# Optimization experiments

Measured on AMD Instinct MI355X. Metric: run time of the kernel, lower is better.

## Reference

```python
import jax, jax.numpy as jnp
import numpy as np

N = 50000      # nodes
E = 800000     # edges
F_NODE = 64
PE = 16
F_EDGE = 16
H = 128        # hidden_dim
L = 4          # num_layers
G = 64         # graphs in batch
NC = 10        # num_classes
BN_EPS = 1e-5


def _bn(h, g, b):
    # BatchNorm1d with batch statistics (deterministic train-style stats, no dropout)
    m = jnp.mean(h, axis=0)
    v = jnp.var(h, axis=0)
    return (h - m) * jax.lax.rsqrt(v + BN_EPS) * g + b


def setup_inputs() -> dict:
    key = jax.random.key(0)
    ks = jax.random.split(key, 16)
    p = lambda k, shape: (jax.random.normal(k, shape, jnp.float32) * 0.05)
    return dict(
        x=jax.random.normal(ks[0], (N, F_NODE), jnp.float32),
        pe=jax.random.normal(ks[1], (N, PE), jnp.float32),
        edge_index=jax.random.randint(ks[2], (2, E), 0, N),
        edge_attr=jax.random.normal(ks[3], (E, F_EDGE), jnp.float32),
        batch=jnp.sort(jax.random.randint(ks[4], (N,), 0, G)),
        W_in=p(ks[5], (F_NODE + PE, H)), b_in=jnp.zeros((H,), jnp.float32),
        We_edge=p(ks[6], (L, F_EDGE, H)), be_edge=jnp.zeros((L, H), jnp.float32),
        eps=jnp.zeros((L,), jnp.float32),
        W1_gin=p(ks[7], (L, H, 2 * H)), b1_gin=jnp.zeros((L, 2 * H), jnp.float32),
        W2_gin=p(ks[8], (L, 2 * H, H)), b2_gin=jnp.zeros((L, H), jnp.float32),
        bn1_g=jnp.ones((L, H), jnp.float32), bn1_b=jnp.zeros((L, H), jnp.float32),
        W1_ffn=p(ks[9], (L, H, 2 * H)), b1_ffn=jnp.zeros((L, 2 * H), jnp.float32),
        W2_ffn=p(ks[10], (L, 2 * H, H)), b2_ffn=jnp.zeros((L, H), jnp.float32),
        bn2_g=jnp.ones((L, H), jnp.float32), bn2_b=jnp.zeros((L, H), jnp.float32),
        W_r1=p(ks[11], (H, H)), b_r1=jnp.zeros((H,), jnp.float32),
        W_r2=p(ks[12], (H, NC)), b_r2=jnp.zeros((NC,), jnp.float32),
    )


def reference(x, pe, edge_index, edge_attr, batch,
              W_in, b_in, We_edge, be_edge, eps,
              W1_gin, b1_gin, W2_gin, b2_gin, bn1_g, bn1_b,
              W1_ffn, b1_ffn, W2_ffn, b2_ffn, bn2_g, bn2_b,
              W_r1, b_r1, W_r2, b_r2):
    src, dst = edge_index[0], edge_index[1]  # PyG: row=source j, col=target i
    # input projection on [x || pe]
    h = jax.nn.relu(jnp.concatenate([x, pe], axis=-1) @ W_in + b_in)  # [N,H]
    for l in range(L):
        # --- GINEConv: msg = relu(x_j + lin_edge(e_ij)); sum-aggregate to target
        e = edge_attr @ We_edge[l] + be_edge[l]                        # [E,H]
        msg = jax.nn.relu(h[src] + e)                                  # gather + fuse
        agg = jax.ops.segment_sum(msg, dst, num_segments=N)           # scatter-add
        z = (1.0 + eps[l]) * h + agg
        z = jax.nn.relu(z @ W1_gin[l] + b1_gin[l]) @ W2_gin[l] + b2_gin[l]
        # --- GNNPlusLayer: BN -> ReLU -> residual (identity proj, in==out)
        z = jax.nn.relu(_bn(z, bn1_g[l], bn1_b[l]))
        z = z + h
        # --- FFN (eval mode): out = lin2(relu(lin1(z))) + z, then BN
        f = jax.nn.relu(z @ W1_ffn[l] + b1_ffn[l]) @ W2_ffn[l] + b2_ffn[l]
        h = _bn(f + z, bn2_g[l], bn2_b[l])
    # --- global mean pool over graphs
    sums = jax.ops.segment_sum(h, batch, num_segments=G)               # [G,H]
    counts = jax.ops.segment_sum(jnp.ones((N,), h.dtype), batch, num_segments=G)
    hg = sums / jnp.maximum(counts, 1.0)[:, None]
    # --- readout MLP (dropout off in eval)
    return jax.nn.relu(hg @ W_r1 + b_r1) @ W_r2 + b_r2                 # [G,NC]
```

## Files before the change

kernel.cpp:

```cpp
#include <hip/hip_runtime.h>
#include <hip/hip_bf16.h>

#define NN 50000
#define NE 800000
#define FIN 80
#define H 128
#define H2 256
#define NG 64
#define NCLS 10
#define BN_EPS 1e-5f
#define NB 196
#define LDK 40
#define LDY 264

typedef __attribute__((ext_vector_type(8))) short bf16x8;
typedef __attribute__((ext_vector_type(8))) unsigned short us8;
typedef __attribute__((ext_vector_type(4))) float f32x4;
typedef __attribute__((ext_vector_type(2))) float f32x2;

__device__ __forceinline__ unsigned short f2b(float f) {
    __hip_bfloat16 h = __float2bfloat16(f);
    return *(unsigned short*)&h;
}
__device__ __forceinline__ float b2f(unsigned short u) {
    unsigned v = (unsigned)u << 16;
    return __uint_as_float(v);
}

__global__ void wprep_all(const float* __restrict__ W1g, const float* __restrict__ W2g,
                          const float* __restrict__ W1f, const float* __restrict__ W2f,
                          unsigned short* __restrict__ wt)
{
    const int idx = blockIdx.x * 256 + threadIdx.x;
    const int m = idx >> 17;
    const int r = idx & 131071;
    const float* W;
    unsigned short* Wt;
    int K, Nn;
    if (m == 0)      { W = W1g; Wt = wt;              K = 128; Nn = 256; }
    else if (m == 1) { W = W2g; Wt = wt + 4 * 65536;  K = 256; Nn = 128; }
    else if (m == 2) { W = W1f; Wt = wt + 8 * 65536;  K = 128; Nn = 256; }
    else             { W = W2f; Wt = wt + 12 * 65536; K = 256; Nn = 128; }
    const int per = K * Nn;
    const int l = r / per;
    const int rr = r - l * per;
    const int k = rr / Nn;
    const int n = rr - k * Nn;
    const float wv = W[r];
    const unsigned short hi = f2b(wv);
    const unsigned short lo = f2b(wv - b2f(hi));
    const int KB = K >> 5;
    const int kb = k >> 5, kk = k & 31;
    unsigned short* base = Wt + (size_t)l * 2 * per;
    base[((size_t)(0 * KB + kb) * Nn + n) * 32 + kk] = hi;
    base[((size_t)(1 * KB + kb) * Nn + n) * 32 + kk] = lo;
}

template<bool ZF>
__global__ __launch_bounds__(256, 3)
void gemm_pair(const void* __restrict__ Ap, const float* __restrict__ hres,
               const unsigned short* __restrict__ Wt1, const unsigned short* __restrict__ Wt2,
               const float* __restrict__ b1, const float* __restrict__ b2,
               const float* __restrict__ statsIn, const float* __restrict__ bng,
               const float* __restrict__ bnb, float* __restrict__ statsOut,
               float* __restrict__ Cout, float inv_n, int M)
{
    __shared__ unsigned short sA[ZF ? 64 : 1][LDK];
    __shared__ unsigned short sy[64][LDY];
    __shared__ float sAB[128];
    __shared__ float sSH[128];

    const int tid = threadIdx.x;
    const int m0 = blockIdx.x * 64;
    const int lane = tid & 63;
    const int w = tid >> 6;
    const int fr = lane & 15;
    const int fq = (lane >> 4) * 8;
    const int crow4 = (lane >> 4) * 4;

    if (ZF) {
#pragma unroll
        for (int rep = 0; rep < 2; ++rep) {
            const int c = lane + rep * 64;
            float su = 0.f, qu = 0.f;
#pragma unroll
            for (int s = 0; s < 8; ++s) {
                su += statsIn[s * 256 + c];
                qu += statsIn[s * 256 + 128 + c];
            }
            const float mean = su * inv_n;
            const float var = qu * inv_n - mean * mean;
            const float a = bng[c] * rsqrtf(var + BN_EPS);
            sAB[c] = a;
            sSH[c] = fmaf(-mean, a, bnb[c]);
        }
    }

    f32x4 acc1[16];
#pragma unroll
    for (int c = 0; c < 16; ++c) acc1[c] = (f32x4)(0.f);

    const int arow = tid >> 2;
    const int akq = (tid & 3) * 8;

    for (int kb = 0; kb < 4; ++kb) {
        bf16x8 a0;
        if (ZF) {
            const int gm = m0 + arow;
            if (gm < M) {
                const float* tf = (const float*)Ap + (size_t)gm * 128 + kb * 32 + akq;
                const float* hf = hres + (size_t)gm * 128 + kb * 32 + akq;
                const float4 t0 = *(const float4*)tf;
                const float4 t1 = *(const float4*)(tf + 4);
                const float4 h0 = *(const float4*)hf;
                const float4 h1 = *(const float4*)(hf + 4);
                const float tv[8] = {t0.x, t0.y, t0.z, t0.w, t1.x, t1.y, t1.z, t1.w};
                const float hv[8] = {h0.x, h0.y, h0.z, h0.w, h1.x, h1.y, h1.z, h1.w};
                us8 p;
#pragma unroll
                for (int i = 0; i < 8; ++i) {
                    const int c = kb * 32 + akq + i;
                    p[i] = f2b(fmaxf(fmaf(tv[i], sAB[c], sSH[c]), 0.f) + hv[i]);
                }
                *(us8*)&sA[arow][akq] = p;
            } else {
                *(float4*)&sA[arow][akq] = make_float4(0.f, 0.f, 0.f, 0.f);
            }
            a0 = *(const bf16x8*)&sA[w * 16 + fr][fq];
        } else {
            const unsigned short* zp = (const unsigned short*)Ap +
                                       (size_t)(m0 + w * 16 + fr) * 128 + kb * 32 + fq;
            a0 = *(const bf16x8*)zp;
        }
#pragma unroll
        for (int nt = 0; nt < 16; ++nt) {
            const bf16x8 bh = *(const bf16x8*)&Wt1[((size_t)(kb) * 256 + nt * 16 + fr) * 32 + fq];
            const bf16x8 bl = *(const bf16x8*)&Wt1[((size_t)(4 + kb) * 256 + nt * 16 + fr) * 32 + fq];
            acc1[nt] = __builtin_amdgcn_mfma_f32_16x16x32_bf16(a0, bh, acc1[nt], 0, 0, 0);
            acc1[nt] = __builtin_amdgcn_mfma_f32_16x16x32_bf16(a0, bl, acc1[nt], 0, 0, 0);
        }
    }

#pragma unroll
    for (int nt = 0; nt < 16; ++nt) {
        const float bb = b1[nt * 16 + fr];
#pragma unroll
        for (int reg = 0; reg < 4; ++reg) {
            const float o = fmaxf(acc1[nt][reg] + bb, 0.f);
            sy[w * 16 + crow4 + reg][nt * 16 + fr] = f2b(o);
        }
    }

    f32x4 acc2[8];
#pragma unroll
    for (int c = 0; c < 8; ++c) acc2[c] = (f32x4)(0.f);

    for (int kb = 0; kb < 8; ++kb) {
        const bf16x8 ya = *(const bf16x8*)&sy[w * 16 + fr][kb * 32 + fq];
#pragma unroll
        for (int ct = 0; ct < 8; ++ct) {
            const bf16x8 bh = *(const bf16x8*)&Wt2[((size_t)(kb) * 128 + ct * 16 + fr) * 32 + fq];
            const bf16x8 bl = *(const bf16x8*)&Wt2[((size_t)(8 + kb) * 128 + ct * 16 + fr) * 32 + fq];
            acc2[ct] = __builtin_amdgcn_mfma_f32_16x16x32_bf16(ya, bh, acc2[ct], 0, 0, 0);
            acc2[ct] = __builtin_amdgcn_mfma_f32_16x16x32_bf16(ya, bl, acc2[ct], 0, 0, 0);
        }
    }

    float s[8], q[8];
#pragma unroll
    for (int c = 0; c < 8; ++c) { s[c] = 0.f; q[c] = 0.f; }
    const int rbase = m0 + w * 16 + crow4;
#pragma unroll
    for (int ct = 0; ct < 8; ++ct) {
        const int gc = ct * 16 + fr;
        const float bb = b2[gc];
#pragma unroll
        for (int reg = 0; reg < 4; ++reg) {
            const int gr = rbase + reg;
            if (gr >= M) continue;
            float o = acc2[ct][reg] + bb;
            if (ZF) {
                const float tv = ((const float*)Ap)[(size_t)gr * 128 + gc];
                const float hv = hres[(size_t)gr * 128 + gc];
                o += fmaxf(fmaf(tv, sAB[gc], sSH[gc]), 0.f) + hv;
            }
            s[ct] += o;
            q[ct] = fmaf(o, o, q[ct]);
            Cout[(size_t)gr * 128 + gc] = o;
        }
    }

#pragma unroll
    for (int c = 0; c < 8; ++c) {
        s[c] += __shfl_xor(s[c], 32, 64); s[c] += __shfl_xor(s[c], 16, 64);
        q[c] += __shfl_xor(q[c], 32, 64); q[c] += __shfl_xor(q[c], 16, 64);
    }
    __syncthreads();
    float* red = (float*)sy;
    if (lane < 16) {
#pragma unroll
        for (int c = 0; c < 8; ++c) {
            red[w * 128 + c * 16 + lane]       = s[c];
            red[512 + w * 128 + c * 16 + lane] = q[c];
        }
    }
    __syncthreads();
    if (tid < 128) {
        const float ss = red[tid] + red[128 + tid] + red[256 + tid] + red[384 + tid];
        const float qq = red[512 + tid] + red[640 + tid] + red[768 + tid] + red[896 + tid];
        float* slab = statsOut + (blockIdx.x & 7) * 256;
        atomicAdd(&slab[tid], ss);
        atomicAdd(&slab[128 + tid], qq);
    }
}

__global__ __launch_bounds__(256, 4)
void inproj_kernel(const float* __restrict__ x, const float* __restrict__ pe,
                   const float* __restrict__ W, const float* __restrict__ bias,
                   float* __restrict__ C, unsigned short* __restrict__ Cb, int M)
{
    __shared__ float aT[16][129];
    __shared__ float wsh[16][129];

    const int tid = threadIdx.x;
    const int m0 = blockIdx.x * 128;
    const int rm = (tid >> 4) * 8;
    const int rn = (tid & 15) * 8;

    float acc[8][8];
#pragma unroll
    for (int i = 0; i < 8; ++i)
#pragma unroll
        for (int j = 0; j < 8; ++j) acc[i][j] = 0.f;

    const int lm = tid & 127;
    const int kq = (tid >> 7) * 8;
    const int wk = tid >> 4;
    const int wj = (tid & 15) * 8;

    for (int k0 = 0; k0 < FIN; k0 += 16) {
        {
            const int gm = m0 + lm;
            const int c = k0 + kq;
            if (gm < M) {
                const float* srcp = (c < 64) ? (x + (size_t)gm * 64 + c)
                                             : (pe + (size_t)gm * 16 + (c - 64));
                const float4 v0 = *(const float4*)srcp;
                const float4 v1 = *(const float4*)(srcp + 4);
                aT[kq + 0][lm] = v0.x; aT[kq + 1][lm] = v0.y;
                aT[kq + 2][lm] = v0.z; aT[kq + 3][lm] = v0.w;
                aT[kq + 4][lm] = v1.x; aT[kq + 5][lm] = v1.y;
                aT[kq + 6][lm] = v1.z; aT[kq + 7][lm] = v1.w;
            } else {
#pragma unroll
                for (int i = 0; i < 8; ++i) aT[kq + i][lm] = 0.f;
            }
        }
        {
#pragma unroll
            for (int j = 0; j < 8; ++j)
                wsh[wk][wj + j] = W[(size_t)(k0 + wk) * H + wj + j];
        }
        __syncthreads();
#pragma unroll
        for (int k = 0; k < 16; ++k) {
            const float av[8] = {aT[k][rm], aT[k][rm + 1], aT[k][rm + 2], aT[k][rm + 3],
                                 aT[k][rm + 4], aT[k][rm + 5], aT[k][rm + 6], aT[k][rm + 7]};
            const float bv[8] = {wsh[k][rn], wsh[k][rn + 1], wsh[k][rn + 2], wsh[k][rn + 3],
                                 wsh[k][rn + 4], wsh[k][rn + 5], wsh[k][rn + 6], wsh[k][rn + 7]};
#pragma unroll
            for (int i = 0; i < 8; ++i)
#pragma unroll
                for (int j = 0; j < 8; ++j)
                    acc[i][j] = fmaf(av[i], bv[j], acc[i][j]);
        }
        __syncthreads();
    }

    float bv[8];
#pragma unroll
    for (int j = 0; j < 8; ++j) bv[j] = bias[rn + j];
#pragma unroll
    for (int i = 0; i < 8; ++i) {
        const int gm = m0 + rm + i;
        if (gm >= M) continue;
        float o[8];
#pragma unroll
        for (int j = 0; j < 8; ++j) o[j] = fmaxf(acc[i][j] + bv[j], 0.f);
        *(float4*)&C[(size_t)gm * H + rn]     = make_float4(o[0], o[1], o[2], o[3]);
        *(float4*)&C[(size_t)gm * H + rn + 4] = make_float4(o[4], o[5], o[6], o[7]);
        us8 pk;
#pragma unroll
        for (int j = 0; j < 8; ++j) pk[j] = f2b(o[j]);
        *(us8*)&Cb[(size_t)gm * H + rn] = pk;
    }
}

__global__ void hist_kernel(const int* __restrict__ ei, int* __restrict__ deg)
{
    const int e = blockIdx.x * 256 + threadIdx.x;
    if (e < NE) atomicAdd(&deg[ei[NE + e]], 1);
}

__global__ void bsum_kernel(const int* __restrict__ deg, int* __restrict__ bsum)
{
    const int tid = threadIdx.x;
    const int i = blockIdx.x * 256 + tid;
    int v = (i < NN) ? deg[i] : 0;
#pragma unroll
    for (int off = 32; off > 0; off >>= 1) v += __shfl_down(v, off, 64);
    __shared__ int ws[4];
    if ((tid & 63) == 0) ws[tid >> 6] = v;
    __syncthreads();
    if (tid == 0) bsum[blockIdx.x] = ws[0] + ws[1] + ws[2] + ws[3];
}

__global__ void bscan_kernel(int* __restrict__ bsum)
{
    __shared__ int sh[256];
    const int tid = threadIdx.x;
    sh[tid] = (tid < NB) ? bsum[tid] : 0;
    __syncthreads();
    for (int off = 1; off < 256; off <<= 1) {
        const int t = (tid >= off) ? sh[tid - off] : 0;
        __syncthreads();
        sh[tid] += t;
        __syncthreads();
    }
    if (tid < NB) bsum[tid] = (tid == 0) ? 0 : sh[tid - 1];
}

__global__ void bwrite_kernel(const int* __restrict__ deg, const int* __restrict__ boff,
                              int* __restrict__ rowptr, int* __restrict__ cursor)
{
    __shared__ int sh[256];
    const int tid = threadIdx.x;
    const int i = blockIdx.x * 256 + tid;
    const int v = (i < NN) ? deg[i] : 0;
    sh[tid] = v;
    __syncthreads();
    for (int off = 1; off < 256; off <<= 1) {
        const int t = (tid >= off) ? sh[tid - off] : 0;
        __syncthreads();
        sh[tid] += t;
        __syncthreads();
    }
    if (i < NN) {
        const int pos = boff[blockIdx.x] + sh[tid] - v;
        rowptr[i] = pos;
        cursor[i] = pos;
    }
    if (blockIdx.x == 0 && tid == 0) rowptr[NN] = NE;
}

__global__ void scat_idx(const int* __restrict__ ei, int* __restrict__ cursor,
                         int* __restrict__ src_s, int* __restrict__ perm)
{
    const int e = blockIdx.x * 256 + threadIdx.x;
    if (e >= NE) return;
    const int pos = atomicAdd(&cursor[ei[NE + e]], 1);
    src_s[pos] = ei[e];
    perm[pos] = e;
}

__global__ void gather_ea(const float* __restrict__ ea, const int* __restrict__ perm,
                          float* __restrict__ ea_s)
{
    const int idx = blockIdx.x * 256 + threadIdx.x;
    const int pos = idx >> 2;
    const int qd = idx & 3;
    const int e = perm[pos];
    *(float4*)&ea_s[(size_t)pos * 16 + qd * 4] = *(const float4*)&ea[(size_t)e * 16 + qd * 4];
}

__global__ __launch_bounds__(256)
void agg_kernel(const float* __restrict__ h, const unsigned short* __restrict__ hb,
                const int* __restrict__ rowptr, const int* __restrict__ src_s,
                const float* __restrict__ ea_s, const float* __restrict__ We,
                const float* __restrict__ be, const float* __restrict__ eps, int l,
                unsigned short* __restrict__ zb)
{
    const int lane = threadIdx.x & 63;
    const int w = threadIdx.x >> 6;
    const int n = blockIdx.x * 4 + w;
    if (n >= NN) return;

    f32x2 wv[16];
#pragma unroll
    for (int k = 0; k < 16; ++k)
        wv[k] = *(const f32x2*)&We[k * H + 2 * lane];
    const f32x2 bev = *(const f32x2*)&be[2 * lane];

    const int beg = __builtin_amdgcn_readfirstlane(rowptr[n]);
    const int end = __builtin_amdgcn_readfirstlane(rowptr[n + 1]);

    const float e1 = 1.0f + eps[l];
    f32x2 acc = (*(const f32x2*)&h[(size_t)n * H + 2 * lane]) * e1;

    for (int i0 = beg; i0 < end; i0 += 16) {
        const int jn = min(16, end - i0);
        int srcs[16];
#pragma unroll
        for (int j = 0; j < 16; ++j)
            srcs[j] = src_s[(i0 + j < end) ? (i0 + j) : (end - 1)];
        unsigned hraw[16];
#pragma unroll
        for (int j = 0; j < 16; ++j)
            hraw[j] = *(const unsigned*)&hb[(size_t)srcs[j] * H + 2 * lane];
#pragma unroll
        for (int j = 0; j < 16; ++j) {
            if (j >= jn) break;
            const float* ar = ea_s + (size_t)(i0 + j) * 16;
            f32x2 s2 = bev;
#pragma unroll
            for (int k = 0; k < 16; ++k)
                s2 = __builtin_elementwise_fma((f32x2)(ar[k]), wv[k], s2);
            f32x2 hv = {__uint_as_float(hraw[j] << 16),
                        __uint_as_float(hraw[j] & 0xffff0000u)};
            f32x2 m = hv + s2;
            m = __builtin_elementwise_max(m, (f32x2)(0.f));
            acc += m;
        }
    }
    const unsigned u = ((unsigned)f2b(acc[1]) << 16) | (unsigned)f2b(acc[0]);
    *(unsigned*)&zb[(size_t)n * H + 2 * lane] = u;
}

__global__ void bn_apply_kernel(const float* __restrict__ u, const float* __restrict__ st,
                                const float* __restrict__ g, const float* __restrict__ b,
                                float* __restrict__ h, unsigned short* __restrict__ hb,
                                float inv_n)
{
    const int i = blockIdx.x * 256 + threadIdx.x;
    const int c = i & (H - 1);
    float su = 0.f, qu = 0.f;
#pragma unroll
    for (int s = 0; s < 8; ++s) { su += st[s * 256 + c]; qu += st[s * 256 + 128 + c]; }
    const float mean = su * inv_n;
    const float var = qu * inv_n - mean * mean;
    const float a = g[c] * rsqrtf(var + BN_EPS);
    const float sh = fmaf(-mean, a, b[c]);
    const float v = fmaf(u[i], a, sh);
    h[i] = v;
    hb[i] = f2b(v);
}

__global__ void pool_kernel(const float* __restrict__ h, const int* __restrict__ batch,
                            float* __restrict__ pool, float* __restrict__ cnt, int n)
{
    const int c = threadIdx.x & (H - 1);
    const int half = threadIdx.x >> 7;
    const int r0 = blockIdx.x * 256 + half * 128;
    if (r0 >= n) return;
    const int rend = min(r0 + 128, n);
    int gprev = batch[r0];
    float acc = 0.f;
    int run = 0;
    for (int r = r0; r < rend; ++r) {
        const int g = batch[r];
        if (g != gprev) {
            atomicAdd(&pool[gprev * H + c], acc);
            if (c == 0) atomicAdd(&cnt[gprev], (float)run);
            acc = 0.f; run = 0; gprev = g;
        }
        acc += h[(size_t)r * H + c];
        run++;
    }
    atomicAdd(&pool[gprev * H + c], acc);
    if (c == 0) atomicAdd(&cnt[gprev], (float)run);
}

__global__ void readout_kernel(const float* __restrict__ pool, const float* __restrict__ cnt,
                               const float* __restrict__ Wr1, const float* __restrict__ br1,
                               const float* __restrict__ Wr2, const float* __restrict__ br2,
                               float* __restrict__ out)
{
    __shared__ float hg[H];
    __shared__ float r1[H];
    const int g = blockIdx.x;
    const int j = threadIdx.x;
    hg[j] = pool[g * H + j] / fmaxf(cnt[g], 1.0f);
    __syncthreads();
    float acc = br1[j];
    for (int k = 0; k < H; ++k) acc = fmaf(hg[k], Wr1[k * H + j], acc);
    r1[j] = fmaxf(acc, 0.f);
    __syncthreads();
    if (j < NCLS) {
        float o = br2[j];
        for (int k = 0; k < H; ++k) o = fmaf(r1[k], Wr2[k * NCLS + j], o);
        out[g * NCLS + j] = o;
    }
}

extern "C" void kernel_launch(void* const* d_in, const int* in_sizes, int n_in,
                              void* d_out, int out_size, void* d_ws, size_t ws_size,
                              hipStream_t stream)
{
    const float* x       = (const float*)d_in[0];
    const float* pe      = (const float*)d_in[1];
    const int*   ei      = (const int*)d_in[2];
    const float* ea      = (const float*)d_in[3];
    const int*   batch   = (const int*)d_in[4];
    const float* W_in    = (const float*)d_in[5];
    const float* b_in    = (const float*)d_in[6];
    const float* We_edge = (const float*)d_in[7];
    const float* be_edge = (const float*)d_in[8];
    const float* eps     = (const float*)d_in[9];
    const float* W1g     = (const float*)d_in[10];
    const float* b1g     = (const float*)d_in[11];
    const float* W2g     = (const float*)d_in[12];
    const float* b2g     = (const float*)d_in[13];
    const float* bn1g    = (const float*)d_in[14];
    const float* bn1b    = (const float*)d_in[15];
    const float* W1f     = (const float*)d_in[16];
    const float* b1f     = (const float*)d_in[17];
    const float* W2f     = (const float*)d_in[18];
    const float* b2f     = (const float*)d_in[19];
    const float* bn2g    = (const float*)d_in[20];
    const float* bn2b    = (const float*)d_in[21];
    const float* Wr1     = (const float*)d_in[22];
    const float* br1     = (const float*)d_in[23];
    const float* Wr2     = (const float*)d_in[24];
    const float* br2     = (const float*)d_in[25];
    float* out = (float*)d_out;

    const size_t NH = (size_t)NN * H;
    float* hbuf  = (float*)d_ws;
    float* tbuf  = hbuf + NH;
    unsigned short* zb = (unsigned short*)(tbuf + NH);
    int*   perm  = (int*)(zb + NH);
    int*   deg   = perm + NE;
    float* stats = (float*)(deg + NN);
    float* pool  = stats + 16384;
    float* cnt   = pool + NG * H;
    int*   rowptr = (int*)(cnt + NG);
    int*   cursor = rowptr + NN + 1;
    int*   bsum   = cursor + NN;
    int*   src_s  = bsum + 256;
    float* ea_s   = (float*)(src_s + NE);
    unsigned short* hb = (unsigned short*)(ea_s + (size_t)NE * 16);
    unsigned short* wt = hb + NH;
    unsigned short* wt1g = wt;
    unsigned short* wt2g = wt + 4 * 65536;
    unsigned short* wt1f = wt + 8 * 65536;
    unsigned short* wt2f = wt + 12 * 65536;

    const dim3 blk(256);
    const dim3 ip_g((NN + 127) / 128, 1);
    const dim3 gp_g((NN + 63) / 64, 1);
    const int ew_grid = (int)(NH / 256);
    const float inv_n = 1.0f / (float)NN;
    const size_t zero_bytes = (size_t)(NN + 16384 + NG * H + NG) * 4;

    wprep_all<<<2048, blk, 0, stream>>>(W1g, W2g, W1f, W2f, wt);

    hipMemsetAsync(deg, 0, zero_bytes, stream);
    hist_kernel<<<(NE + 255) / 256, blk, 0, stream>>>(ei, deg);
    bsum_kernel<<<NB, blk, 0, stream>>>(deg, bsum);
    bscan_kernel<<<1, blk, 0, stream>>>(bsum);
    bwrite_kernel<<<NB, blk, 0, stream>>>(deg, bsum, rowptr, cursor);
    scat_idx<<<(NE + 255) / 256, blk, 0, stream>>>(ei, cursor, src_s, perm);
    gather_ea<<<(NE * 4) / 256, blk, 0, stream>>>(ea, perm, ea_s);

    inproj_kernel<<<ip_g, blk, 0, stream>>>(x, pe, W_in, b_in, hbuf, hb, NN);

    for (int l = 0; l < 4; ++l) {
        float* s1 = stats + (size_t)l * 4096;
        float* s2 = s1 + 2048;

        agg_kernel<<<(NN + 3) / 4, blk, 0, stream>>>(hbuf, hb, rowptr, src_s, ea_s,
                                                     We_edge + (size_t)l * 16 * H,
                                                     be_edge + (size_t)l * H, eps, l, zb);

        gemm_pair<false><<<gp_g, blk, 0, stream>>>(
            zb, nullptr, wt1g + (size_t)l * 65536, wt2g + (size_t)l * 65536,
            b1g + (size_t)l * H2, b2g + (size_t)l * H,
            nullptr, nullptr, nullptr, s1, tbuf, inv_n, NN);

        gemm_pair<true><<<gp_g, blk, 0, stream>>>(
            tbuf, hbuf, wt1f + (size_t)l * 65536, wt2f + (size_t)l * 65536,
            b1f + (size_t)l * H2, b2f + (size_t)l * H,
            s1, bn1g + (size_t)l * H, bn1b + (size_t)l * H, s2, tbuf, inv_n, NN);

        bn_apply_kernel<<<ew_grid, blk, 0, stream>>>(tbuf, s2, bn2g + (size_t)l * H,
                                                     bn2b + (size_t)l * H, hbuf, hb, inv_n);
    }

    pool_kernel<<<(NN + 255) / 256, blk, 0, stream>>>(hbuf, batch, pool, cnt, NN);
    readout_kernel<<<NG, H, 0, stream>>>(pool, cnt, Wr1, br1, Wr2, br2, out);
}
```

Before: 1.388 ms.

## Double gemm_pair row tile to 128 so each wave reuses weight fragments twice

Each wave now computes two 16-row MFMA tiles instead of one, so every global weight fragment load (hi/lo split bf16) feeds two MFMAs. The block covers 128 rows, shared buffers double, and the grid halves. The aim is to halve weight-load traffic per output row. The cost is doubled accumulator registers (launch bounds lowered to 2 blocks per SM), more shared memory and fewer blocks to spread across the GPU. One leftover redundant sA read is dead code.

```diff
diff --git a/kernel.cpp b/kernel.cpp
--- a/kernel.cpp
+++ b/kernel.cpp
@@ -57,7 +57,7 @@
 }
 
 template<bool ZF>
-__global__ __launch_bounds__(256, 3)
+__global__ __launch_bounds__(256, 2)
 void gemm_pair(const void* __restrict__ Ap, const float* __restrict__ hres,
                const unsigned short* __restrict__ Wt1, const unsigned short* __restrict__ Wt2,
                const float* __restrict__ b1, const float* __restrict__ b2,
@@ -65,13 +65,13 @@
                const float* __restrict__ bnb, float* __restrict__ statsOut,
                float* __restrict__ Cout, float inv_n, int M)
 {
-    __shared__ unsigned short sA[ZF ? 64 : 1][LDK];
-    __shared__ unsigned short sy[64][LDY];
+    __shared__ unsigned short sA[ZF ? 128 : 1][LDK];
+    __shared__ unsigned short sy[128][LDY];
     __shared__ float sAB[128];
     __shared__ float sSH[128];
 
     const int tid = threadIdx.x;
-    const int m0 = blockIdx.x * 64;
+    const int m0 = blockIdx.x * 128;
     const int lane = tid & 63;
     const int w = tid >> 6;
     const int fr = lane & 15;
@@ -96,48 +96,67 @@
         }
     }
 
-    f32x4 acc1[16];
-#pragma unroll
-    for (int c = 0; c < 16; ++c) acc1[c] = (f32x4)(0.f);
-
-    const int arow = tid >> 2;
-    const int akq = (tid & 3) * 8;
+    f32x4 acc1[2][16];
+#pragma unroll
+    for (int r = 0; r < 2; ++r)
+#pragma unroll
+        for (int c = 0; c < 16; ++c) acc1[r][c] = (f32x4)(0.f);
+
+    const int arow = tid >> 1;
+    const int akh = (tid & 1) * 16;
+    const int gm = m0 + arow;
 
     for (int kb = 0; kb < 4; ++kb) {
-        bf16x8 a0;
+        bf16x8 a0, a1;
         if (ZF) {
-            const int gm = m0 + arow;
             if (gm < M) {
-                const float* tf = (const float*)Ap + (size_t)gm * 128 + kb * 32 + akq;
-                const float* hf = hres + (size_t)gm * 128 + kb * 32 + akq;
+                const float* tf = (const float*)Ap + (size_t)gm * 128 + kb * 32 + akh;
+                const float* hf = hres + (size_t)gm * 128 + kb * 32 + akh;
                 const float4 t0 = *(const float4*)tf;
                 const float4 t1 = *(const float4*)(tf + 4);
+                const float4 t2 = *(const float4*)(tf + 8);
+                const float4 t3 = *(const float4*)(tf + 12);
                 const float4 h0 = *(const float4*)hf;
                 const float4 h1 = *(const float4*)(hf + 4);
-                const float tv[8] = {t0.x, t0.y, t0.z, t0.w, t1.x, t1.y, t1.z, t1.w};
-                const float hv[8] = {h0.x, h0.y, h0.z, h0.w, h1.x, h1.y, h1.z, h1.w};
-                us8 p;
+                const float4 h2 = *(const float4*)(hf + 8);
+                const float4 h3 = *(const float4*)(hf + 12);
+                const float tv[16] = {t0.x, t0.y, t0.z, t0.w, t1.x, t1.y, t1.z, t1.w,
+                                      t2.x, t2.y, t2.z, t2.w, t3.x, t3.y, t3.z, t3.w};
+                const float hv[16] = {h0.x, h0.y, h0.z, h0.w, h1.x, h1.y, h1.z, h1.w,
+                                      h2.x, h2.y, h2.z, h2.w, h3.x, h3.y, h3.z, h3.w};
+                us8 p0, p1;
 #pragma unroll
                 for (int i = 0; i < 8; ++i) {
-                    const int c = kb * 32 + akq + i;
-                    p[i] = f2b(fmaxf(fmaf(tv[i], sAB[c], sSH[c]), 0.f) + hv[i]);
+                    const int c = kb * 32 + akh + i;
+                    const int c2 = c + 8;
+                    p0[i] = f2b(fmaxf(fmaf(tv[i], sAB[c], sSH[c]), 0.f) + hv[i]);
+                    p1[i] = f2b(fmaxf(fmaf(tv[8 + i], sAB[c2], sSH[c2]), 0.f) + hv[8 + i]);
                 }
-                *(us8*)&sA[arow][akq] = p;
+                *(us8*)&sA[arow][akh]     = p0;
+                *(us8*)&sA[arow][akh + 8] = p1;
             } else {
-                *(float4*)&sA[arow][akq] = make_float4(0.f, 0.f, 0.f, 0.f);
+                *(float4*)&sA[arow][akh]     = make_float4(0.f, 0.f, 0.f, 0.f);
+                *(float4*)&sA[arow][akh + 8] = make_float4(0.f, 0.f, 0.f, 0.f);
             }
-            a0 = *(const bf16x8*)&sA[w * 16 + fr][fq];
+            a0 = *(const bf16x8*)&sA[w * 32 + fr][kb * 32 + akh - akh + fq];
+            a0 = *(const bf16x8*)&sA[w * 32 + fr][fq];
+            a1 = *(const bf16x8*)&sA[w * 32 + 16 + fr][fq];
         } else {
-            const unsigned short* zp = (const unsigned short*)Ap +
-                                       (size_t)(m0 + w * 16 + fr) * 128 + kb * 32 + fq;
-            a0 = *(const bf16x8*)zp;
+            const unsigned short* z0 = (const unsigned short*)Ap +
+                                       (size_t)(m0 + w * 32 + fr) * 128 + kb * 32 + fq;
+            const unsigned short* z1 = (const unsigned short*)Ap +
+                                       (size_t)(m0 + w * 32 + 16 + fr) * 128 + kb * 32 + fq;
+            a0 = *(const bf16x8*)z0;
+            a1 = *(const bf16x8*)z1;
         }
 #pragma unroll
         for (int nt = 0; nt < 16; ++nt) {
             const bf16x8 bh = *(const bf16x8*)&Wt1[((size_t)(kb) * 256 + nt * 16 + fr) * 32 + fq];
             const bf16x8 bl = *(const bf16x8*)&Wt1[((size_t)(4 + kb) * 256 + nt * 16 + fr) * 32 + fq];
-            acc1[nt] = __builtin_amdgcn_mfma_f32_16x16x32_bf16(a0, bh, acc1[nt], 0, 0, 0);
-            acc1[nt] = __builtin_amdgcn_mfma_f32_16x16x32_bf16(a0, bl, acc1[nt], 0, 0, 0);
+            acc1[0][nt] = __builtin_amdgcn_mfma_f32_16x16x32_bf16(a0, bh, acc1[0][nt], 0, 0, 0);
+            acc1[0][nt] = __builtin_amdgcn_mfma_f32_16x16x32_bf16(a0, bl, acc1[0][nt], 0, 0, 0);
+            acc1[1][nt] = __builtin_amdgcn_mfma_f32_16x16x32_bf16(a1, bh, acc1[1][nt], 0, 0, 0);
+            acc1[1][nt] = __builtin_amdgcn_mfma_f32_16x16x32_bf16(a1, bl, acc1[1][nt], 0, 0, 0);
         }
     }
 
@@ -145,48 +164,60 @@
     for (int nt = 0; nt < 16; ++nt) {
         const float bb = b1[nt * 16 + fr];
 #pragma unroll
-        for (int reg = 0; reg < 4; ++reg) {
-            const float o = fmaxf(acc1[nt][reg] + bb, 0.f);
-            sy[w * 16 + crow4 + reg][nt * 16 + fr] = f2b(o);
-        }
-    }
-
-    f32x4 acc2[8];
-#pragma unroll
-    for (int c = 0; c < 8; ++c) acc2[c] = (f32x4)(0.f);
+        for (int r = 0; r < 2; ++r) {
+            const int row0 = w * 32 + r * 16 + crow4;
+#pragma unroll
+            for (int reg = 0; reg < 4; ++reg) {
+                const float o = fmaxf(acc1[r][nt][reg] + bb, 0.f);
+                sy[row0 + reg][nt * 16 + fr] = f2b(o);
+            }
+        }
+    }
+
+    f32x4 acc2[2][8];
+#pragma unroll
+    for (int r = 0; r < 2; ++r)
+#pragma unroll
+        for (int c = 0; c < 8; ++c) acc2[r][c] = (f32x4)(0.f);
 
     for (int kb = 0; kb < 8; ++kb) {
-        const bf16x8 ya = *(const bf16x8*)&sy[w * 16 + fr][kb * 32 + fq];
+        const bf16x8 ya0 = *(const bf16x8*)&sy[w * 32 + fr][kb * 32 + fq];
+        const bf16x8 ya1 = *(const bf16x8*)&sy[w * 32 + 16 + fr][kb * 32 + fq];
 #pragma unroll
         for (int ct = 0; ct < 8; ++ct) {
             const bf16x8 bh = *(const bf16x8*)&Wt2[((size_t)(kb) * 128 + ct * 16 + fr) * 32 + fq];
             const bf16x8 bl = *(const bf16x8*)&Wt2[((size_t)(8 + kb) * 128 + ct * 16 + fr) * 32 + fq];
-            acc2[ct] = __builtin_amdgcn_mfma_f32_16x16x32_bf16(ya, bh, acc2[ct], 0, 0, 0);
-            acc2[ct] = __builtin_amdgcn_mfma_f32_16x16x32_bf16(ya, bl, acc2[ct], 0, 0, 0);
+            acc2[0][ct] = __builtin_amdgcn_mfma_f32_16x16x32_bf16(ya0, bh, acc2[0][ct], 0, 0, 0);
+            acc2[0][ct] = __builtin_amdgcn_mfma_f32_16x16x32_bf16(ya0, bl, acc2[0][ct], 0, 0, 0);
+            acc2[1][ct] = __builtin_amdgcn_mfma_f32_16x16x32_bf16(ya1, bh, acc2[1][ct], 0, 0, 0);
+            acc2[1][ct] = __builtin_amdgcn_mfma_f32_16x16x32_bf16(ya1, bl, acc2[1][ct], 0, 0, 0);
         }
     }
 
     float s[8], q[8];
 #pragma unroll
     for (int c = 0; c < 8; ++c) { s[c] = 0.f; q[c] = 0.f; }
-    const int rbase = m0 + w * 16 + crow4;
-#pragma unroll
-    for (int ct = 0; ct < 8; ++ct) {
-        const int gc = ct * 16 + fr;
-        const float bb = b2[gc];
-#pragma unroll
-        for (int reg = 0; reg < 4; ++reg) {
-            const int gr = rbase + reg;
-            if (gr >= M) continue;
-            float o = acc2[ct][reg] + bb;
-            if (ZF) {
-                const float tv = ((const float*)Ap)[(size_t)gr * 128 + gc];
-                const float hv = hres[(size_t)gr * 128 + gc];
-                o += fmaxf(fmaf(tv, sAB[gc], sSH[gc]), 0.f) + hv;
+#pragma unroll
+    for (int r = 0; r < 2; ++r) {
+        const int rbase = m0 + w * 32 + r * 16 + crow4;
+#pragma unroll
+        for (int ct = 0; ct < 8; ++ct) {
+            const int gc = ct * 16 + fr;
+            const float bb = b2[gc];
+#pragma unroll
+            for (int reg = 0; reg < 4; ++reg) {
+                const int gr = rbase + reg;
+                if (gr >= M) continue;
+                float o = acc2[r][ct][reg] + bb;
+                if (ZF) {
+                    const float tv = ((const float*)Ap)[(size_t)gr * 128 + gc];
+                    const float hv = hres[(size_t)gr * 128 + gc];
+                    o += fmaxf(fmaf(tv, sAB[gc], sSH[gc]), 0.f) + hv;
+                }
+                s[ct] += o;
+                q[ct] = fmaf(o, o, q[ct]);
+                Cout[(size_t)gr * 128 + gc] = o;
             }
-            s[ct] += o;
-            q[ct] = fmaf(o, o, q[ct]);
-            Cout[(size_t)gr * 128 + gc] = o;
         }
     }
 
@@ -547,7 +578,7 @@
 
     const dim3 blk(256);
     const dim3 ip_g((NN + 127) / 128, 1);
-    const dim3 gp_g((NN + 63) / 64, 1);
+    const dim3 gp_g((NN + 127) / 128, 1);
     const int ew_grid = (int)(NH / 256);
     const float inv_n = 1.0f / (float)NN;
     const size_t zero_bytes = (size_t)(NN + 16384 + NG * H + NG) * 4;
```

Result: faster. 1.145 ms (-17.5%).
